# Kernel tuning notes

Measured on AMD Instinct MI355X. Metric: run time of the kernel, lower is better.

Reference implementation:

```python
import jax, jax.numpy as jnp
import numpy as np
from jax.scipy.linalg import expm

U_SHAPE = (4, 32, 16, 16, 16, 3, 3)   # [mu, t, x, y, z, 3, 3]
W_SHAPE = (8, 32, 16, 16, 16, 3, 3)   # [feature, t, x, y, z, 3, 3]


def setup_inputs() -> dict:
    key = jax.random.key(0)
    k = jax.random.split(key, 5)
    return {
        "U_re": jax.random.normal(k[0], U_SHAPE, jnp.float32),
        "U_im": jax.random.normal(k[1], U_SHAPE, jnp.float32),
        "W_re": jax.random.normal(k[2], W_SHAPE, jnp.float32),
        "W_im": jax.random.normal(k[3], W_SHAPE, jnp.float32),
        "ah_weights": jax.random.normal(k[4], (4, W_SHAPE[0]), jnp.float32),
    }


def reference(U_re, U_im, W_re, W_im, ah_weights):
    U = (U_re + 1j * U_im).astype(jnp.complex64)
    W = (W_re + 1j * W_im).astype(jnp.complex64)

    # anti-hermitian part: W - W^dagger
    W_adj = jnp.conj(jnp.swapaxes(W, -1, -2))
    A = W - W_adj
    # traceless projection
    tr = jnp.trace(A, axis1=-2, axis2=-1)  # [i,t,x,y,z]
    A = A - (tr / 3.0)[..., None, None] * jnp.eye(3, dtype=A.dtype)

    # exponent: (1j*w) contracted with (-1j*A) == w contracted with A
    E = jnp.einsum('ui,itxyzab->utxyzab', ah_weights.astype(A.dtype), A)

    # batched 3x3 matrix exponential over the whole lattice
    E_flat = E.reshape(-1, 3, 3)
    expE = jax.vmap(expm)(E_flat).reshape(E.shape)

    # apply to gauge links: exp(...) @ U
    return jnp.einsum('utxyzij,utxyzjk->utxyzik', expE, U)
```

## Files before the change

### kernel.cpp

```cpp
#include <hip/hip_runtime.h>
#include <math.h>

#define NSITES 131072

struct cplx { float re, im; };

__device__ __forceinline__ cplx cadd(cplx a, cplx b) { return {a.re + b.re, a.im + b.im}; }
__device__ __forceinline__ cplx cmul(cplx a, cplx b) {
    return { fmaf(a.re, b.re, -(a.im * b.im)), fmaf(a.re, b.im, a.im * b.re) };
}

struct __attribute__((aligned(4))) f3 { float x, y, z; };
__device__ __forceinline__ f3 ld3(const float* __restrict__ p) { return *(const f3*)p; }
__device__ __forceinline__ void ld9(const float* __restrict__ p, float* r) {
    f3 a = *(const f3*)p, b = *(const f3*)(p + 3), c = *(const f3*)(p + 6);
    r[0] = a.x; r[1] = a.y; r[2] = a.z;
    r[3] = b.x; r[4] = b.y; r[5] = b.z;
    r[6] = c.x; r[7] = c.y; r[8] = c.z;
}

#define ECOL(m0, m1, m2, v0, v1, v2) do { \
    v0.re = fmaf(-ed0, m0.im, fmaf(er01, m1.re, fmaf(-ei01, m1.im, fmaf(er02, m2.re, -(ei02 * m2.im))))); \
    v0.im = fmaf( ed0, m0.re, fmaf(er01, m1.im, fmaf( ei01, m1.re, fmaf(er02, m2.im,  (ei02 * m2.re))))); \
    v1.re = fmaf(-er01, m0.re, fmaf(-ei01, m0.im, fmaf(-ed1, m1.im, fmaf(er12, m2.re, -(ei12 * m2.im))))); \
    v1.im = fmaf(-er01, m0.im, fmaf( ei01, m0.re, fmaf( ed1, m1.re, fmaf(er12, m2.im,  (ei12 * m2.re))))); \
    v2.re = fmaf(-er02, m0.re, fmaf(-ei02, m0.im, fmaf(-er12, m1.re, fmaf(-ei12, m1.im, -(ed2 * m2.im))))); \
    v2.im = fmaf(-er02, m0.im, fmaf( ei02, m0.re, fmaf(-er12, m1.im, fmaf( ei12, m1.re,  (ed2 * m2.re))))); \
} while (0)

#define OCOMB(m, v, z) \
    fmaf(g0.re, m.re, fmaf(-g0.im, m.im, fmaf(g1.re, v.re, fmaf(-g1.im, v.im, \
    fmaf(g2.re, z.re, -(g2.im * z.im))))))

__global__ __launch_bounds__(256, 4) void lge_exp_kernel(
    const float* __restrict__ U_re, const float* __restrict__ U_im,
    const float* __restrict__ W_re, const float* __restrict__ W_im,
    const float* __restrict__ ahw,  float* __restrict__ out)
{
    const int gid   = blockIdx.x * 256 + threadIdx.x;
    const int gsite = gid >> 2;
    const int mu    = gid & 3;

    const float4* ahw4 = (const float4*)ahw;
    float4 wlo = ahw4[mu * 2], whi = ahw4[mu * 2 + 1];
    const float wfv[8] = { wlo.x, wlo.y, wlo.z, wlo.w, whi.x, whi.y, whi.z, whi.w };

    const size_t sb = (size_t)gsite * 9;

    float er01 = 0.f, er02 = 0.f, er12 = 0.f;
    float a0=0.f,a1=0.f,a2=0.f,a3=0.f,a4=0.f,a5=0.f,a6=0.f,a7=0.f,a8=0.f;
    #pragma unroll
    for (int f = 0; f < 8; f++) {
        const float* pr = W_re + (size_t)f * (NSITES * 9) + sb;
        const float* pi = W_im + (size_t)f * (NSITES * 9) + sb;
        f3 q = ld3(pr + 1);
        f3 s = ld3(pr + 5);
        float wi[9];
        ld9(pi, wi);
        const float wf = wfv[f];
        er01 = fmaf(wf, q.x - q.z, er01);
        er02 = fmaf(wf, q.y - s.y, er02);
        er12 = fmaf(wf, s.x - s.z, er12);
        a0 = fmaf(wf, wi[0], a0); a1 = fmaf(wf, wi[1], a1); a2 = fmaf(wf, wi[2], a2);
        a3 = fmaf(wf, wi[3], a3); a4 = fmaf(wf, wi[4], a4); a5 = fmaf(wf, wi[5], a5);
        a6 = fmaf(wf, wi[6], a6); a7 = fmaf(wf, wi[7], a7); a8 = fmaf(wf, wi[8], a8);
    }

    const int ub = (mu * NSITES + gsite) * 9;
    float ur[9], ui[9];
    ld9(U_re + ub, ur);
    ld9(U_im + ub, ui);

    const float ei01 = a1 + a3, ei02 = a2 + a6, ei12 = a5 + a7;
    const float t3  = (a0 + a4 + a8) * (2.f / 3.f);
    const float ed0 = fmaf(2.f, a0, -t3);
    const float ed1 = fmaf(2.f, a4, -t3);
    const float ed2 = fmaf(2.f, a8, -t3);

    float r2 = fmaf(er01, er01, fmaf(er02, er02, fmaf(er12, er12,
               fmaf(ei01, ei01, fmaf(ei02, ei02, ei12 * ei12)))));
    r2 = fmaf(2.f, r2, fmaf(ed0, ed0, fmaf(ed1, ed1, ed2 * ed2)));

    const float n01 = fmaf(ei01, ei01, er01 * er01);
    const float n02 = fmaf(ei02, ei02, er02 * er02);
    const float n12 = fmaf(ei12, ei12, er12 * er12);
    const float zre = fmaf(ei01, ei12, -(er01 * er12));
    const float zim = -fmaf(ei01, er12, er01 * ei12);
    const float detH = ed0 * ed1 * ed2
                     + 2.f * fmaf(zre, ei02, -(zim * er02))
                     - fmaf(ed0, n12, fmaf(ed1, n02, ed2 * n01));

    int e; (void)frexpf(r2, &e);
    int sc = (e <= -2) ? 0 : min(1 + ((e + 1) >> 1), 40);
    const float inv  = __int_as_float((127 - sc) << 23);
    const float inv2 = inv * inv;
    const float px   = -0.5f * r2 * inv2;
    const float qxi  = -detH * (inv2 * inv);

    cplx T0 = {1.f, 0.f}, T1 = {0.f, 0.f}, T2 = {0.f, 0.f};
    cplx S0 = {1.f, 0.f}, S1 = {0.f, 0.f}, S2 = {0.f, 0.f};
    #pragma unroll
    for (int n = 1; n <= 10; n++) {
        float c  = 1.f / (float)n;
        float qc = qxi * c;
        cplx nT0 = { -qc * T2.im, qc * T2.re };
        cplx nT1 = { c * fmaf(px, T2.re, T0.re), c * fmaf(px, T2.im, T0.im) };
        cplx nT2 = { c * T1.re, c * T1.im };
        T0 = nT0; T1 = nT1; T2 = nT2;
        S0 = cadd(S0, T0); S1 = cadd(S1, T1); S2 = cadd(S2, T2);
    }

    const float q2 = 2.f * qxi;
    for (int k = 0; k < sc; k++) {
        cplx f0 = S0, f1 = S1, f2 = S2;
        cplx f12 = cmul(f1, f2);
        cplx f01 = cmul(f0, f1);
        cplx f02 = cmul(f0, f2);
        float f00re = fmaf(f0.re, f0.re, -(f0.im * f0.im)), f00im = 2.f * f0.re * f0.im;
        float f11re = fmaf(f1.re, f1.re, -(f1.im * f1.im)), f11im = 2.f * f1.re * f1.im;
        float f22re = fmaf(f2.re, f2.re, -(f2.im * f2.im)), f22im = 2.f * f2.re * f2.im;
        S0.re = fmaf(-q2, f12.im, f00re);
        S0.im = fmaf( q2, f12.re, f00im);
        S1.re = fmaf(-qxi, f22im, 2.f * fmaf(px, f12.re, f01.re));
        S1.im = fmaf( qxi, f22re, 2.f * fmaf(px, f12.im, f01.im));
        S2.re = fmaf(px, f22re, fmaf(2.f, f02.re, f11re));
        S2.im = fmaf(px, f22im, fmaf(2.f, f02.im, f11im));
    }
    const cplx g0 = S0;
    const cplx g1 = { S1.re * inv,  S1.im * inv  };
    const cplx g2 = { S2.re * inv2, S2.im * inv2 };

    float o[9];
    #pragma unroll
    for (int b = 0; b < 3; b++) {
        cplx m0 = { ur[b],     ui[b]     };
        cplx m1 = { ur[3 + b], ui[3 + b] };
        cplx m2 = { ur[6 + b], ui[6 + b] };
        cplx v0, v1, v2, z0, z1, z2;
        ECOL(m0, m1, m2, v0, v1, v2);
        ECOL(v0, v1, v2, z0, z1, z2);
        o[b]     = OCOMB(m0, v0, z0);
        o[3 + b] = OCOMB(m1, v1, z1);
        o[6 + b] = OCOMB(m2, v2, z2);
    }

    float* ob = out + ub;
    *(f3*)(ob)     = { o[0], o[1], o[2] };
    *(f3*)(ob + 3) = { o[3], o[4], o[5] };
    *(f3*)(ob + 6) = { o[6], o[7], o[8] };
}

extern "C" void kernel_launch(void* const* d_in, const int* in_sizes, int n_in,
                              void* d_out, int out_size, void* d_ws, size_t ws_size,
                              hipStream_t stream) {
    const float* U_re = (const float*)d_in[0];
    const float* U_im = (const float*)d_in[1];
    const float* W_re = (const float*)d_in[2];
    const float* W_im = (const float*)d_in[3];
    const float* ahw  = (const float*)d_in[4];
    float* out = (float*)d_out;
    lge_exp_kernel<<<dim3(NSITES * 4 / 256), dim3(256), 0, stream>>>(
        U_re, U_im, W_re, W_im, ahw, out);
}
```

Baseline: 145.5 us.

## Split W feature loads across the four mu lanes and share via ds_swizzle

Before, each of the four threads working on one site (one per mu) loaded all 8 features of W, so every W value was fetched four times. Now each lane loads only features mu and mu+4, precomputes the 9 needed combinations, and broadcasts them to its neighbouring lanes with ds_swizzle quad-broadcast patterns before accumulating. This cuts redundant global/L1 load instructions by roughly four times. In exchange it adds 72 swizzle operations per thread, which go through the LDS crossbar and cost some latency.

```diff
diff --git a/kernel.cpp b/kernel.cpp
--- a/kernel.cpp
+++ b/kernel.cpp
@@ -18,6 +18,20 @@
     r[3] = b.x; r[4] = b.y; r[5] = b.z;
     r[6] = c.x; r[7] = c.y; r[8] = c.z;
 }
+
+#define SWZ(imm, x) __int_as_float(__builtin_amdgcn_ds_swizzle(__float_as_int(x), imm))
+
+#define ACCF(arr, wf, imm) do { \
+    er01 = fmaf(wf, SWZ(imm, arr[0]), er01); \
+    er02 = fmaf(wf, SWZ(imm, arr[1]), er02); \
+    er12 = fmaf(wf, SWZ(imm, arr[2]), er12); \
+    si01 = fmaf(wf, SWZ(imm, arr[3]), si01); \
+    si02 = fmaf(wf, SWZ(imm, arr[4]), si02); \
+    si12 = fmaf(wf, SWZ(imm, arr[5]), si12); \
+    dd0  = fmaf(wf, SWZ(imm, arr[6]), dd0); \
+    dd4  = fmaf(wf, SWZ(imm, arr[7]), dd4); \
+    dd8  = fmaf(wf, SWZ(imm, arr[8]), dd8); \
+} while (0)
 
 #define ECOL(m0, m1, m2, v0, v1, v2) do { \
     v0.re = fmaf(-ed0, m0.im, fmaf(er01, m1.re, fmaf(-ei01, m1.im, fmaf(er02, m2.re, -(ei02 * m2.im))))); \
@@ -47,35 +61,45 @@
 
     const size_t sb = (size_t)gsite * 9;
 
-    float er01 = 0.f, er02 = 0.f, er12 = 0.f;
-    float a0=0.f,a1=0.f,a2=0.f,a3=0.f,a4=0.f,a5=0.f,a6=0.f,a7=0.f,a8=0.f;
-    #pragma unroll
-    for (int f = 0; f < 8; f++) {
-        const float* pr = W_re + (size_t)f * (NSITES * 9) + sb;
-        const float* pi = W_im + (size_t)f * (NSITES * 9) + sb;
-        f3 q = ld3(pr + 1);
-        f3 s = ld3(pr + 5);
-        float wi[9];
-        ld9(pi, wi);
-        const float wf = wfv[f];
-        er01 = fmaf(wf, q.x - q.z, er01);
-        er02 = fmaf(wf, q.y - s.y, er02);
-        er12 = fmaf(wf, s.x - s.z, er12);
-        a0 = fmaf(wf, wi[0], a0); a1 = fmaf(wf, wi[1], a1); a2 = fmaf(wf, wi[2], a2);
-        a3 = fmaf(wf, wi[3], a3); a4 = fmaf(wf, wi[4], a4); a5 = fmaf(wf, wi[5], a5);
-        a6 = fmaf(wf, wi[6], a6); a7 = fmaf(wf, wi[7], a7); a8 = fmaf(wf, wi[8], a8);
-    }
+    const float* prA = W_re + (size_t)mu * (NSITES * 9) + sb;
+    const float* piA = W_im + (size_t)mu * (NSITES * 9) + sb;
+    const float* prB = W_re + (size_t)(mu + 4) * (NSITES * 9) + sb;
+    const float* piB = W_im + (size_t)(mu + 4) * (NSITES * 9) + sb;
+
+    f3 qA = ld3(prA + 1), sA = ld3(prA + 5);
+    float iA[9]; ld9(piA, iA);
+    f3 qB = ld3(prB + 1), sB = ld3(prB + 5);
+    float iB[9]; ld9(piB, iB);
 
     const int ub = (mu * NSITES + gsite) * 9;
     float ur[9], ui[9];
     ld9(U_re + ub, ur);
     ld9(U_im + ub, ui);
 
-    const float ei01 = a1 + a3, ei02 = a2 + a6, ei12 = a5 + a7;
-    const float t3  = (a0 + a4 + a8) * (2.f / 3.f);
-    const float ed0 = fmaf(2.f, a0, -t3);
-    const float ed1 = fmaf(2.f, a4, -t3);
-    const float ed2 = fmaf(2.f, a8, -t3);
+    float fa[9] = { qA.x - qA.z,  qA.y - sA.y,  sA.x - sA.z,
+                    iA[1] + iA[3], iA[2] + iA[6], iA[5] + iA[7],
+                    iA[0], iA[4], iA[8] };
+    float fb[9] = { qB.x - qB.z,  qB.y - sB.y,  sB.x - sB.z,
+                    iB[1] + iB[3], iB[2] + iB[6], iB[5] + iB[7],
+                    iB[0], iB[4], iB[8] };
+
+    float er01 = 0.f, er02 = 0.f, er12 = 0.f;
+    float si01 = 0.f, si02 = 0.f, si12 = 0.f;
+    float dd0 = 0.f, dd4 = 0.f, dd8 = 0.f;
+    ACCF(fa, wfv[0], 0x1C);
+    ACCF(fa, wfv[1], 0x3C);
+    ACCF(fa, wfv[2], 0x5C);
+    ACCF(fa, wfv[3], 0x7C);
+    ACCF(fb, wfv[4], 0x1C);
+    ACCF(fb, wfv[5], 0x3C);
+    ACCF(fb, wfv[6], 0x5C);
+    ACCF(fb, wfv[7], 0x7C);
+
+    const float ei01 = si01, ei02 = si02, ei12 = si12;
+    const float t3  = (dd0 + dd4 + dd8) * (2.f / 3.f);
+    const float ed0 = fmaf(2.f, dd0, -t3);
+    const float ed1 = fmaf(2.f, dd4, -t3);
+    const float ed2 = fmaf(2.f, dd8, -t3);
 
     float r2 = fmaf(er01, er01, fmaf(er02, er02, fmaf(er12, er12,
                fmaf(ei01, ei01, fmaf(ei02, ei02, ei12 * ei12)))));
```

New measurement: 144.1 us. No clear change (-1.0%).

## Share W loads across mu lanes via ds_swizzle and process two sites per thread

Applied to the files above, without the earlier changes.

Before this change, each of the 4 mu-lanes of a site loaded all 8 W features, so every W value was read four times. Now each lane loads only 2 features (mu and mu+4), pre-reduces them to the 9 needed components, and gets the other lanes' values through ds_swizzle broadcasts inside each group of 4 lanes. Each thread also handles two sites (sA and sA+HALFS), and the grid is halved to match, which adds instruction-level parallelism. The intent is to cut redundant W load traffic. The cost is swizzle instructions and higher register pressure, which may reduce occupancy.

```diff
diff --git a/kernel.cpp b/kernel.cpp
--- a/kernel.cpp
+++ b/kernel.cpp
@@ -2,6 +2,8 @@
 #include <math.h>
 
 #define NSITES 131072
+#define HALFS  (NSITES / 2)
+#define PL     (NSITES * 9)
 
 struct cplx { float re, im; };
 
@@ -19,76 +21,48 @@
     r[6] = c.x; r[7] = c.y; r[8] = c.z;
 }
 
-#define ECOL(m0, m1, m2, v0, v1, v2) do { \
-    v0.re = fmaf(-ed0, m0.im, fmaf(er01, m1.re, fmaf(-ei01, m1.im, fmaf(er02, m2.re, -(ei02 * m2.im))))); \
-    v0.im = fmaf( ed0, m0.re, fmaf(er01, m1.im, fmaf( ei01, m1.re, fmaf(er02, m2.im,  (ei02 * m2.re))))); \
-    v1.re = fmaf(-er01, m0.re, fmaf(-ei01, m0.im, fmaf(-ed1, m1.im, fmaf(er12, m2.re, -(ei12 * m2.im))))); \
-    v1.im = fmaf(-er01, m0.im, fmaf( ei01, m0.re, fmaf( ed1, m1.re, fmaf(er12, m2.im,  (ei12 * m2.re))))); \
-    v2.re = fmaf(-er02, m0.re, fmaf(-ei02, m0.im, fmaf(-er12, m1.re, fmaf(-ei12, m1.im, -(ed2 * m2.im))))); \
-    v2.im = fmaf(-er02, m0.im, fmaf( ei02, m0.re, fmaf(-er12, m1.im, fmaf( ei12, m1.re,  (ed2 * m2.re))))); \
-} while (0)
-
-#define OCOMB(m, v, z) \
-    fmaf(g0.re, m.re, fmaf(-g0.im, m.im, fmaf(g1.re, v.re, fmaf(-g1.im, v.im, \
-    fmaf(g2.re, z.re, -(g2.im * z.im))))))
-
-__global__ __launch_bounds__(256, 4) void lge_exp_kernel(
-    const float* __restrict__ U_re, const float* __restrict__ U_im,
-    const float* __restrict__ W_re, const float* __restrict__ W_im,
-    const float* __restrict__ ahw,  float* __restrict__ out)
-{
-    const int gid   = blockIdx.x * 256 + threadIdx.x;
-    const int gsite = gid >> 2;
-    const int mu    = gid & 3;
-
-    const float4* ahw4 = (const float4*)ahw;
-    float4 wlo = ahw4[mu * 2], whi = ahw4[mu * 2 + 1];
-    const float wfv[8] = { wlo.x, wlo.y, wlo.z, wlo.w, whi.x, whi.y, whi.z, whi.w };
-
-    const size_t sb = (size_t)gsite * 9;
-
-    float er01 = 0.f, er02 = 0.f, er12 = 0.f;
-    float a0=0.f,a1=0.f,a2=0.f,a3=0.f,a4=0.f,a5=0.f,a6=0.f,a7=0.f,a8=0.f;
+template<int IMM>
+__device__ __forceinline__ void accf(const float* a, float wf, float* acc) {
     #pragma unroll
-    for (int f = 0; f < 8; f++) {
-        const float* pr = W_re + (size_t)f * (NSITES * 9) + sb;
-        const float* pi = W_im + (size_t)f * (NSITES * 9) + sb;
-        f3 q = ld3(pr + 1);
-        f3 s = ld3(pr + 5);
-        float wi[9];
-        ld9(pi, wi);
-        const float wf = wfv[f];
-        er01 = fmaf(wf, q.x - q.z, er01);
-        er02 = fmaf(wf, q.y - s.y, er02);
-        er12 = fmaf(wf, s.x - s.z, er12);
-        a0 = fmaf(wf, wi[0], a0); a1 = fmaf(wf, wi[1], a1); a2 = fmaf(wf, wi[2], a2);
-        a3 = fmaf(wf, wi[3], a3); a4 = fmaf(wf, wi[4], a4); a5 = fmaf(wf, wi[5], a5);
-        a6 = fmaf(wf, wi[6], a6); a7 = fmaf(wf, wi[7], a7); a8 = fmaf(wf, wi[8], a8);
-    }
-
-    const int ub = (mu * NSITES + gsite) * 9;
-    float ur[9], ui[9];
-    ld9(U_re + ub, ur);
-    ld9(U_im + ub, ui);
-
-    const float ei01 = a1 + a3, ei02 = a2 + a6, ei12 = a5 + a7;
-    const float t3  = (a0 + a4 + a8) * (2.f / 3.f);
-    const float ed0 = fmaf(2.f, a0, -t3);
-    const float ed1 = fmaf(2.f, a4, -t3);
-    const float ed2 = fmaf(2.f, a8, -t3);
-
-    float r2 = fmaf(er01, er01, fmaf(er02, er02, fmaf(er12, er12,
-               fmaf(ei01, ei01, fmaf(ei02, ei02, ei12 * ei12)))));
-    r2 = fmaf(2.f, r2, fmaf(ed0, ed0, fmaf(ed1, ed1, ed2 * ed2)));
-
-    const float n01 = fmaf(ei01, ei01, er01 * er01);
-    const float n02 = fmaf(ei02, ei02, er02 * er02);
-    const float n12 = fmaf(ei12, ei12, er12 * er12);
-    const float zre = fmaf(ei01, ei12, -(er01 * er12));
-    const float zim = -fmaf(ei01, er12, er01 * ei12);
-    const float detH = ed0 * ed1 * ed2
-                     + 2.f * fmaf(zre, ei02, -(zim * er02))
-                     - fmaf(ed0, n12, fmaf(ed1, n02, ed2 * n01));
+    for (int m = 0; m < 9; m++)
+        acc[m] = fmaf(wf,
+            __int_as_float(__builtin_amdgcn_ds_swizzle(__float_as_int(a[m]), IMM)),
+            acc[m]);
+}
+
+__device__ __forceinline__ void prered(f3 q, f3 s, const float* wi, float* fr) {
+    fr[0] = q.x - q.z;     fr[1] = q.y - s.y;     fr[2] = s.x - s.z;
+    fr[3] = wi[1] + wi[3]; fr[4] = wi[2] + wi[6]; fr[5] = wi[5] + wi[7];
+    fr[6] = wi[0];         fr[7] = wi[4];         fr[8] = wi[8];
+}
+
+struct Edof { float er01, er02, er12, ei01, ei02, ei12, ed0, ed1, ed2; };
+
+__device__ __forceinline__ Edof make_edof(const float* acc) {
+    Edof E;
+    E.er01 = acc[0]; E.er02 = acc[1]; E.er12 = acc[2];
+    E.ei01 = acc[3]; E.ei02 = acc[4]; E.ei12 = acc[5];
+    float t3 = (acc[6] + acc[7] + acc[8]) * (2.f / 3.f);
+    E.ed0 = fmaf(2.f, acc[6], -t3);
+    E.ed1 = fmaf(2.f, acc[7], -t3);
+    E.ed2 = fmaf(2.f, acc[8], -t3);
+    return E;
+}
+
+__device__ __forceinline__ void expm_coeffs(const Edof& E, cplx& g0o, cplx& g1o, cplx& g2o)
+{
+    float r2 = fmaf(E.er01, E.er01, fmaf(E.er02, E.er02, fmaf(E.er12, E.er12,
+               fmaf(E.ei01, E.ei01, fmaf(E.ei02, E.ei02, E.ei12 * E.ei12)))));
+    r2 = fmaf(2.f, r2, fmaf(E.ed0, E.ed0, fmaf(E.ed1, E.ed1, E.ed2 * E.ed2)));
+
+    const float n01 = fmaf(E.ei01, E.ei01, E.er01 * E.er01);
+    const float n02 = fmaf(E.ei02, E.ei02, E.er02 * E.er02);
+    const float n12 = fmaf(E.ei12, E.ei12, E.er12 * E.er12);
+    const float zre = fmaf(E.ei01, E.ei12, -(E.er01 * E.er12));
+    const float zim = -fmaf(E.ei01, E.er12, E.er01 * E.ei12);
+    const float detH = E.ed0 * E.ed1 * E.ed2
+                     + 2.f * fmaf(zre, E.ei02, -(zim * E.er02))
+                     - fmaf(E.ed0, n12, fmaf(E.ed1, n02, E.ed2 * n01));
 
     int e; (void)frexpf(r2, &e);
     int sc = (e <= -2) ? 0 : min(1 + ((e + 1) >> 1), 40);
@@ -126,10 +100,31 @@
         S2.re = fmaf(px, f22re, fmaf(2.f, f02.re, f11re));
         S2.im = fmaf(px, f22im, fmaf(2.f, f02.im, f11im));
     }
-    const cplx g0 = S0;
-    const cplx g1 = { S1.re * inv,  S1.im * inv  };
-    const cplx g2 = { S2.re * inv2, S2.im * inv2 };
-
+    g0o = S0;
+    g1o = { S1.re * inv,  S1.im * inv  };
+    g2o = { S2.re * inv2, S2.im * inv2 };
+}
+
+__device__ __forceinline__ void ecol(const Edof& E, cplx m0, cplx m1, cplx m2,
+                                     cplx& v0, cplx& v1, cplx& v2)
+{
+    v0.re = fmaf(-E.ed0, m0.im, fmaf(E.er01, m1.re, fmaf(-E.ei01, m1.im, fmaf(E.er02, m2.re, -(E.ei02 * m2.im)))));
+    v0.im = fmaf( E.ed0, m0.re, fmaf(E.er01, m1.im, fmaf( E.ei01, m1.re, fmaf(E.er02, m2.im,  (E.ei02 * m2.re)))));
+    v1.re = fmaf(-E.er01, m0.re, fmaf(-E.ei01, m0.im, fmaf(-E.ed1, m1.im, fmaf(E.er12, m2.re, -(E.ei12 * m2.im)))));
+    v1.im = fmaf(-E.er01, m0.im, fmaf( E.ei01, m0.re, fmaf( E.ed1, m1.re, fmaf(E.er12, m2.im,  (E.ei12 * m2.re)))));
+    v2.re = fmaf(-E.er02, m0.re, fmaf(-E.ei02, m0.im, fmaf(-E.er12, m1.re, fmaf(-E.ei12, m1.im, -(E.ed2 * m2.im)))));
+    v2.im = fmaf(-E.er02, m0.im, fmaf( E.ei02, m0.re, fmaf(-E.er12, m1.im, fmaf( E.ei12, m1.re,  (E.ed2 * m2.re)))));
+}
+
+__device__ __forceinline__ float ocomb(cplx g0, cplx g1, cplx g2, cplx m, cplx v, cplx z) {
+    return fmaf(g0.re, m.re, fmaf(-g0.im, m.im, fmaf(g1.re, v.re, fmaf(-g1.im, v.im,
+           fmaf(g2.re, z.re, -(g2.im * z.im))))));
+}
+
+__device__ __forceinline__ void apply_store(const Edof& E, cplx g0, cplx g1, cplx g2,
+                                            const float* ur, const float* ui,
+                                            float* __restrict__ ob)
+{
     float o[9];
     #pragma unroll
     for (int b = 0; b < 3; b++) {
@@ -137,17 +132,79 @@
         cplx m1 = { ur[3 + b], ui[3 + b] };
         cplx m2 = { ur[6 + b], ui[6 + b] };
         cplx v0, v1, v2, z0, z1, z2;
-        ECOL(m0, m1, m2, v0, v1, v2);
-        ECOL(v0, v1, v2, z0, z1, z2);
-        o[b]     = OCOMB(m0, v0, z0);
-        o[3 + b] = OCOMB(m1, v1, z1);
-        o[6 + b] = OCOMB(m2, v2, z2);
+        ecol(E, m0, m1, m2, v0, v1, v2);
+        ecol(E, v0, v1, v2, z0, z1, z2);
+        o[b]     = ocomb(g0, g1, g2, m0, v0, z0);
+        o[3 + b] = ocomb(g0, g1, g2, m1, v1, z1);
+        o[6 + b] = ocomb(g0, g1, g2, m2, v2, z2);
     }
-
-    float* ob = out + ub;
     *(f3*)(ob)     = { o[0], o[1], o[2] };
     *(f3*)(ob + 3) = { o[3], o[4], o[5] };
     *(f3*)(ob + 6) = { o[6], o[7], o[8] };
+}
+
+__global__ __launch_bounds__(256, 4) void lge_exp_kernel(
+    const float* __restrict__ U_re, const float* __restrict__ U_im,
+    const float* __restrict__ W_re, const float* __restrict__ W_im,
+    const float* __restrict__ ahw,  float* __restrict__ out)
+{
+    const int gid = blockIdx.x * 256 + threadIdx.x;
+    const int sA  = gid >> 2;
+    const int mu  = gid & 3;
+    const int sB  = sA + HALFS;
+
+    const float4* ahw4 = (const float4*)ahw;
+    float4 wlo = ahw4[mu * 2], whi = ahw4[mu * 2 + 1];
+    const float wfv[8] = { wlo.x, wlo.y, wlo.z, wlo.w, whi.x, whi.y, whi.z, whi.w };
+
+    const float* WrLo = W_re + (size_t)mu * PL;
+    const float* WiLo = W_im + (size_t)mu * PL;
+    const float* WrHi = W_re + (size_t)(mu + 4) * PL;
+    const float* WiHi = W_im + (size_t)(mu + 4) * PL;
+    const size_t bA = (size_t)sA * 9, bB = (size_t)sB * 9;
+
+    f3 qAl = ld3(WrLo + bA + 1), sAl = ld3(WrLo + bA + 5);
+    f3 qAh = ld3(WrHi + bA + 1), sAh = ld3(WrHi + bA + 5);
+    f3 qBl = ld3(WrLo + bB + 1), sBl = ld3(WrLo + bB + 5);
+    f3 qBh = ld3(WrHi + bB + 1), sBh = ld3(WrHi + bB + 5);
+    float iAl[9]; ld9(WiLo + bA, iAl);
+    float iAh[9]; ld9(WiHi + bA, iAh);
+    float iBl[9]; ld9(WiLo + bB, iBl);
+    float iBh[9]; ld9(WiHi + bB, iBh);
+
+    float faA[9], fbA[9], faB[9], fbB[9];
+    prered(qAl, sAl, iAl, faA);
+    prered(qAh, sAh, iAh, fbA);
+    prered(qBl, sBl, iBl, faB);
+    prered(qBh, sBh, iBh, fbB);
+
+    float accA[9] = {0.f,0.f,0.f,0.f,0.f,0.f,0.f,0.f,0.f};
+    float accB[9] = {0.f,0.f,0.f,0.f,0.f,0.f,0.f,0.f,0.f};
+    accf<0x1C>(faA, wfv[0], accA); accf<0x3C>(faA, wfv[1], accA);
+    accf<0x5C>(faA, wfv[2], accA); accf<0x7C>(faA, wfv[3], accA);
+    accf<0x1C>(fbA, wfv[4], accA); accf<0x3C>(fbA, wfv[5], accA);
+    accf<0x5C>(fbA, wfv[6], accA); accf<0x7C>(fbA, wfv[7], accA);
+    accf<0x1C>(faB, wfv[0], accB); accf<0x3C>(faB, wfv[1], accB);
+    accf<0x5C>(faB, wfv[2], accB); accf<0x7C>(faB, wfv[3], accB);
+    accf<0x1C>(fbB, wfv[4], accB); accf<0x3C>(fbB, wfv[5], accB);
+    accf<0x5C>(fbB, wfv[6], accB); accf<0x7C>(fbB, wfv[7], accB);
+
+    const Edof EA = make_edof(accA);
+    const Edof EB = make_edof(accB);
+
+    const size_t ubA = ((size_t)mu * NSITES + sA) * 9;
+    float urA[9], uiA[9];
+    ld9(U_re + ubA, urA); ld9(U_im + ubA, uiA);
+    cplx g0A, g1A, g2A;
+    expm_coeffs(EA, g0A, g1A, g2A);
+    apply_store(EA, g0A, g1A, g2A, urA, uiA, out + ubA);
+
+    const size_t ubB = ((size_t)mu * NSITES + sB) * 9;
+    float urB[9], uiB[9];
+    ld9(U_re + ubB, urB); ld9(U_im + ubB, uiB);
+    cplx g0B, g1B, g2B;
+    expm_coeffs(EB, g0B, g1B, g2B);
+    apply_store(EB, g0B, g1B, g2B, urB, uiB, out + ubB);
 }
 
 extern "C" void kernel_launch(void* const* d_in, const int* in_sizes, int n_in,
@@ -159,6 +216,6 @@
     const float* W_im = (const float*)d_in[3];
     const float* ahw  = (const float*)d_in[4];
     float* out = (float*)d_out;
-    lge_exp_kernel<<<dim3(NSITES * 4 / 256), dim3(256), 0, stream>>>(
+    lge_exp_kernel<<<dim3(NSITES * 4 / 2 / 256), dim3(256), 0, stream>>>(
         U_re, U_im, W_re, W_im, ahw, out);
 }
```

Result: slower. 157.2 us (+8.1%).
